# Kernel optimization log

Measured on AMD Instinct MI355X. Metric: run time of the kernel, lower is better.

## Reference

```python
import jax, jax.numpy as jnp
import numpy as np

D_MODEL = 1024
D_FF = 4096
N_HEADS = 16
EPS = 1e-5


def setup_inputs() -> dict:
    key = jax.random.key(0)
    ks = jax.random.split(key, 12)
    s = 0.02
    inp = {
        "x": jax.random.normal(ks[0], (4, 2048, D_MODEL), dtype=jnp.float32),
        "Wq": jax.random.normal(ks[1], (D_MODEL, D_MODEL), dtype=jnp.float32) * s,
        "bq": jnp.zeros((D_MODEL,), jnp.float32),
        "Wk": jax.random.normal(ks[2], (D_MODEL, D_MODEL), dtype=jnp.float32) * s,
        "bk": jnp.zeros((D_MODEL,), jnp.float32),
        "Wv": jax.random.normal(ks[3], (D_MODEL, D_MODEL), dtype=jnp.float32) * s,
        "bv": jnp.zeros((D_MODEL,), jnp.float32),
        "Wo": jax.random.normal(ks[4], (D_MODEL, D_MODEL), dtype=jnp.float32) * s,
        "bo": jnp.zeros((D_MODEL,), jnp.float32),
        "ln1_g": jnp.ones((D_MODEL,), jnp.float32),
        "ln1_b": jnp.zeros((D_MODEL,), jnp.float32),
        "ln2_g": jnp.ones((D_MODEL,), jnp.float32),
        "ln2_b": jnp.zeros((D_MODEL,), jnp.float32),
        "W1": jax.random.normal(ks[5], (D_MODEL, D_FF), dtype=jnp.float32) * s,
        "b1": jnp.zeros((D_FF,), jnp.float32),
        "W2": jax.random.normal(ks[6], (D_FF, D_MODEL), dtype=jnp.float32) * s,
        "b2": jnp.zeros((D_MODEL,), jnp.float32),
    }
    return inp


def _layernorm(x, g, b):
    mu = jnp.mean(x, axis=-1, keepdims=True)
    var = jnp.mean(jnp.square(x - mu), axis=-1, keepdims=True)
    return (x - mu) * jax.lax.rsqrt(var + EPS) * g + b


def _block(x, Wq, bq, Wk, bk, Wv, bv, Wo, bo, ln1_g, ln1_b, ln2_g, ln2_b, W1, b1, W2, b2):
    B, S, D = x.shape
    H = N_HEADS
    dk = D // H
    # --- sub_layer1: LN -> MHA ---
    h = _layernorm(x, ln1_g, ln1_b)
    q = (h @ Wq + bq).reshape(B, S, H, dk).transpose(0, 2, 1, 3)  # [B,H,S,dk]
    k = (h @ Wk + bk).reshape(B, S, H, dk).transpose(0, 2, 1, 3)
    v = (h @ Wv + bv).reshape(B, S, H, dk).transpose(0, 2, 1, 3)
    scores = jnp.einsum('bhqd,bhkd->bhqk', q, k) / jnp.sqrt(jnp.float32(dk))
    attn = jax.nn.softmax(scores, axis=-1)
    o = jnp.einsum('bhqk,bhkd->bhqd', attn, v)  # [B,H,S,dk]
    o = o.transpose(0, 2, 1, 3).reshape(B, S, D)
    x = x + (o @ Wo + bo)
    # --- sub_layer2: LN -> MLP (exact GELU) ---
    h = _layernorm(x, ln2_g, ln2_b)
    h = jax.nn.gelu(h @ W1 + b1, approximate=False)
    x = x + (h @ W2 + b2)
    return x


def reference(x, Wq, bq, Wk, bk, Wv, bv, Wo, bo, ln1_g, ln1_b, ln2_g, ln2_b, W1, b1, W2, b2):
    return _block(x, Wq, bq, Wk, bk, Wv, bv, Wo, bo, ln1_g, ln1_b, ln2_g, ln2_b, W1, b1, W2, b2)
```

## Files before the change

### kernel.cpp

```cpp
#include <hip/hip_runtime.h>
#include <hip/hip_bf16.h>
#include <math.h>

#define DM   1024
#define DFF  4096
#define NHEAD 16
#define DKH  64
#define SEQ  2048
#define NBATCH 4
#define NTOK 8192

typedef __attribute__((ext_vector_type(8))) __bf16 bf16x8;
typedef __attribute__((ext_vector_type(8))) short short8;
typedef __attribute__((ext_vector_type(4))) float f32x4;
typedef __attribute__((ext_vector_type(16))) float f32x16;
typedef __attribute__((ext_vector_type(4))) unsigned int u32x4;
typedef __attribute__((ext_vector_type(4))) unsigned short ushort4v;

__device__ __forceinline__ unsigned short f2bf(float f) {
    unsigned u = __builtin_bit_cast(unsigned, f);
    u += 0x7fffu + ((u >> 16) & 1u);
    return (unsigned short)(u >> 16);
}

__device__ __forceinline__ void gload_lds16(const void* g, void* l) {
    __builtin_amdgcn_global_load_lds(
        (const __attribute__((address_space(1))) unsigned int*)g,
        (__attribute__((address_space(3))) unsigned int*)l, 16, 0, 0);
}

__global__ __launch_bounds__(256) void transpose_cvt(
        const float* __restrict__ src, unsigned short* __restrict__ dst, int R, int C) {
    __shared__ unsigned short tile[32][33];
    const int c0 = blockIdx.x * 32, r0 = blockIdx.y * 32;
    const int tx = threadIdx.x & 31, ty = threadIdx.x >> 5;
    #pragma unroll
    for (int j = 0; j < 32; j += 8)
        tile[ty + j][tx] = f2bf(src[(size_t)(r0 + ty + j) * C + (c0 + tx)]);
    __syncthreads();
    #pragma unroll
    for (int j = 0; j < 32; j += 8)
        dst[(size_t)(c0 + ty + j) * R + (r0 + tx)] = tile[tx][ty + j];
}

__global__ __launch_bounds__(256) void concat_bias(
        const float* __restrict__ a, const float* __restrict__ b,
        const float* __restrict__ c, float* __restrict__ out) {
    int i = blockIdx.x * 256 + threadIdx.x;
    out[i] = (i < 1024) ? a[i] : (i < 2048 ? b[i - 1024] : c[i - 2048]);
}

__global__ __launch_bounds__(256) void ln_kernel(
        const float* __restrict__ x, const float* __restrict__ g,
        const float* __restrict__ b, unsigned short* __restrict__ out) {
    const int row = blockIdx.x, t = threadIdx.x;
    const float4 v = ((const float4*)(x + (size_t)row * DM))[t];
    float s1 = v.x + v.y + v.z + v.w;
    float s2 = v.x * v.x + v.y * v.y + v.z * v.z + v.w * v.w;
    #pragma unroll
    for (int off = 32; off > 0; off >>= 1) {
        s1 += __shfl_xor(s1, off, 64);
        s2 += __shfl_xor(s2, off, 64);
    }
    __shared__ float w1[4], w2[4];
    const int wid = t >> 6, lane = t & 63;
    if (lane == 0) { w1[wid] = s1; w2[wid] = s2; }
    __syncthreads();
    s1 = w1[0] + w1[1] + w1[2] + w1[3];
    s2 = w2[0] + w2[1] + w2[2] + w2[3];
    const float mu = s1 * (1.0f / DM);
    const float rs = rsqrtf(s2 * (1.0f / DM) - mu * mu + 1e-5f);
    const float4 gv = ((const float4*)g)[t];
    const float4 bv = ((const float4*)b)[t];
    ushort4v o;
    o[0] = f2bf((v.x - mu) * rs * gv.x + bv.x);
    o[1] = f2bf((v.y - mu) * rs * gv.y + bv.y);
    o[2] = f2bf((v.z - mu) * rs * gv.z + bv.z);
    o[3] = f2bf((v.w - mu) * rs * gv.w + bv.w);
    *(ushort4v*)(out + (size_t)row * DM + t * 4) = o;
}

template<int EP>
__global__ __launch_bounds__(256) void gemm_bf16(
        const unsigned short* __restrict__ A, const unsigned short* __restrict__ BT,
        const float* __restrict__ bias, const float* __restrict__ res,
        void* __restrict__ outp, int M, int N, int K) {
    const int lane = threadIdx.x & 63;
    const int wid  = threadIdx.x >> 6;
    const int m0 = blockIdx.y * 128;
    const int n0 = blockIdx.x * 128;
    __shared__ short As[128 * 32];
    __shared__ short Bs[128 * 32];
    f32x4 acc[4][4] = {};
    const int wm = wid >> 1, wn = wid & 1;
    const int srow = lane >> 2;
    const int scol = (lane & 3) << 3;

    for (int k0 = 0; k0 < K; k0 += 32) {
        __syncthreads();
        #pragma unroll
        for (int i = 0; i < 2; ++i) {
            const int rt = (wid * 2 + i) * 16;
            gload_lds16(A  + (size_t)(m0 + rt + srow) * K + k0 + scol, &As[(wid * 2 + i) * 512]);
            gload_lds16(BT + (size_t)(n0 + rt + srow) * K + k0 + scol, &Bs[(wid * 2 + i) * 512]);
        }
        __syncthreads();
        bf16x8 af[4], bfr[4];
        #pragma unroll
        for (int mi = 0; mi < 4; ++mi)
            af[mi] = *(const bf16x8*)&As[(wm * 64 + mi * 16 + (lane & 15)) * 32 + ((lane >> 4) << 3)];
        #pragma unroll
        for (int ni = 0; ni < 4; ++ni)
            bfr[ni] = *(const bf16x8*)&Bs[(wn * 64 + ni * 16 + (lane & 15)) * 32 + ((lane >> 4) << 3)];
        #pragma unroll
        for (int mi = 0; mi < 4; ++mi)
            #pragma unroll
            for (int ni = 0; ni < 4; ++ni)
                acc[mi][ni] = __builtin_amdgcn_mfma_f32_16x16x32_bf16(af[mi], bfr[ni], acc[mi][ni], 0, 0, 0);
    }

    const int r_base = m0 + wm * 64 + ((lane >> 4) << 2);
    const int c_base = n0 + wn * 64 + (lane & 15);

    if (EP == 4) {
        unsigned short* qP = (unsigned short*)outp;
        unsigned short* kP = qP + (size_t)NTOK * 1024;
        unsigned short* vP = qP + (size_t)2 * NTOK * 1024;
        const int b  = m0 >> 11;
        const int sb = (m0 & 2047) + wm * 64 + ((lane >> 4) << 2);
        #pragma unroll
        for (int ni = 0; ni < 4; ++ni) {
            const int col = c_base + ni * 16;
            const int which = col >> 10;
            const int h = (col >> 6) & 15;
            const int d = col & 63;
            const float bv = bias[col];
            const size_t bh = (size_t)(b * NHEAD + h);
            if (which < 2) {
                unsigned short* dst = (which ? kP : qP) + bh * SEQ * 64 + d;
                #pragma unroll
                for (int mi = 0; mi < 4; ++mi)
                    #pragma unroll
                    for (int i = 0; i < 4; ++i)
                        dst[(size_t)(sb + mi * 16 + i) * 64] = f2bf(acc[mi][ni][i] + bv);
            } else {
                unsigned short* dst = vP + bh * SEQ * 64;
                #pragma unroll
                for (int mi = 0; mi < 4; ++mi) {
                    const int s0 = sb + mi * 16;
                    ushort4v o;
                    #pragma unroll
                    for (int i = 0; i < 4; ++i) o[i] = f2bf(acc[mi][ni][i] + bv);
                    *(ushort4v*)(dst + (s0 >> 5) * 2048 + d * 32 + (s0 & 31)) = o;
                }
            }
        }
        return;
    }

    #pragma unroll
    for (int ni = 0; ni < 4; ++ni) {
        const int col = c_base + ni * 16;
        const float bv = bias[col];
        #pragma unroll
        for (int mi = 0; mi < 4; ++mi) {
            #pragma unroll
            for (int i = 0; i < 4; ++i) {
                const int row = r_base + mi * 16 + i;
                const size_t idx = (size_t)row * N + col;
                float v = acc[mi][ni][i] + bv;
                if (EP == 1 || EP == 3) v += res[idx];
                if (EP == 2) v = 0.5f * v * (1.0f + erff(v * 0.70710678118f));
                if (EP == 0 || EP == 2) ((unsigned short*)outp)[idx] = f2bf(v);
                else                    ((float*)outp)[idx] = v;
            }
        }
    }
}

__global__ __launch_bounds__(256, 4) void attn_kernel(
        const unsigned short* __restrict__ qP, const unsigned short* __restrict__ kP,
        const unsigned short* __restrict__ vP, unsigned short* __restrict__ o) {
    const int lane = threadIdx.x & 63;
    const int wid  = threadIdx.x >> 6;
    const int l31  = lane & 31;
    const int hi   = lane >> 5;
    const int bh = blockIdx.y;
    const int b = bh >> 4, h = bh & 15;
    const int q0 = blockIdx.x * 128 + wid * 32;

    __shared__ short Ks[2][2048];
    __shared__ short Vs[2][2048];
    __shared__ float lsum[4][32];

    bf16x8 qf[4];
    {
        const unsigned short* qp = qP + ((size_t)bh * SEQ + q0 + l31) * 64 + hi * 8;
        #pragma unroll
        for (int s = 0; s < 4; ++s) qf[s] = *(const bf16x8*)(qp + 16 * s);
    }

    const int krow  = wid * 8 + (lane >> 3);
    const int k_src = krow * 64 + (((lane & 7) ^ (lane >> 3)) << 3);
    const int vrow  = wid * 16 + (lane >> 2);
    const int v_src = vrow * 32 + (((lane & 3) ^ ((vrow >> 1) & 3)) << 3);
    const unsigned short* kb = kP + (size_t)bh * SEQ * 64 + k_src;
    const unsigned short* vb = vP + (size_t)bh * SEQ * 64 + v_src;
    short* ksd = &Ks[0][0] + wid * 512;
    short* vsd = &Vs[0][0] + wid * 512;

    auto STAGE = [&](int buf, int kv0) {
        gload_lds16(kb + (size_t)kv0 * 64, ksd + buf * 2048);
        gload_lds16(vb + (size_t)(kv0 >> 5) * 2048, vsd + buf * 2048);
    };

    STAGE(0, 0);
    asm volatile("s_waitcnt vmcnt(0)" ::: "memory");
    __builtin_amdgcn_s_barrier();

    f32x16 oacc0 = {}, oacc1 = {};
    float m_r = -1e30f, l_r = 0.0f;
    const float CE = 0.18033688011f;

    for (int kv0 = 0; kv0 < SEQ; kv0 += 32) {
        const int cur = (kv0 >> 5) & 1;
        if (kv0 + 32 < SEQ) STAGE(cur ^ 1, kv0 + 32);

        const short* kc = &Ks[cur][0];
        const short* vc = &Vs[cur][0];
        bf16x8 kf[4], vf[2][2];
        #pragma unroll
        for (int s = 0; s < 4; ++s)
            kf[s] = *(const bf16x8*)(kc + l31 * 64 + (((2 * s + hi) ^ (l31 & 7)) << 3));
        #pragma unroll
        for (int s = 0; s < 2; ++s)
            #pragma unroll
            for (int n = 0; n < 2; ++n) {
                const int d = l31 + 32 * n;
                vf[s][n] = *(const bf16x8*)(vc + d * 32 + (((2 * s + hi) ^ ((d >> 1) & 3)) << 3));
            }

        f32x16 S = {};
        #pragma unroll
        for (int s = 0; s < 4; ++s)
            S = __builtin_amdgcn_mfma_f32_32x32x16_bf16(kf[s], qf[s], S, 0, 0, 0);

        float t8[8];
        #pragma unroll
        for (int j = 0; j < 8; ++j) t8[j] = fmaxf(S[j], S[j + 8]);
        float tm = fmaxf(fmaxf(fmaxf(t8[0], t8[4]), fmaxf(t8[1], t8[5])),
                         fmaxf(fmaxf(t8[2], t8[6]), fmaxf(t8[3], t8[7])));
        tm = fmaxf(tm, __shfl_xor(tm, 32, 64));
        if (!__all(tm - m_r <= 44.0f)) {
            const float mn = fmaxf(m_r, tm);
            const float es = exp2f((m_r - mn) * CE);
            l_r *= es;
            #pragma unroll
            for (int r = 0; r < 16; ++r) { oacc0[r] *= es; oacc1[r] *= es; }
            m_r = mn;
        }
        float p[16];
        #pragma unroll
        for (int r = 0; r < 16; ++r) p[r] = exp2f((S[r] - m_r) * CE);
        float a8[8];
        #pragma unroll
        for (int j = 0; j < 8; ++j) a8[j] = p[j] + p[j + 8];
        float rs = ((a8[0] + a8[4]) + (a8[1] + a8[5])) + ((a8[2] + a8[6]) + (a8[3] + a8[7]));
        rs += __shfl_xor(rs, 32, 64);
        l_r += rs;

        unsigned pk[8];
        #pragma unroll
        for (int i = 0; i < 8; ++i) {
            unsigned rr;
            asm("v_cvt_pk_bf16_f32 %0, %1, %2" : "=v"(rr) : "v"(p[2 * i]), "v"(p[2 * i + 1]));
            pk[i] = rr;
        }
        asm volatile("v_permlane32_swap_b32 %0, %1" : "+v"(pk[0]), "+v"(pk[2]));
        asm volatile("v_permlane32_swap_b32 %0, %1" : "+v"(pk[1]), "+v"(pk[3]));
        asm volatile("v_permlane32_swap_b32 %0, %1" : "+v"(pk[4]), "+v"(pk[6]));
        asm volatile("v_permlane32_swap_b32 %0, %1" : "+v"(pk[5]), "+v"(pk[7]));
        const bf16x8 A0 = __builtin_bit_cast(bf16x8, (u32x4){pk[0], pk[1], pk[2], pk[3]});
        const bf16x8 A1 = __builtin_bit_cast(bf16x8, (u32x4){pk[4], pk[5], pk[6], pk[7]});

        oacc0 = __builtin_amdgcn_mfma_f32_32x32x16_bf16(A0, vf[0][0], oacc0, 0, 0, 0);
        oacc1 = __builtin_amdgcn_mfma_f32_32x32x16_bf16(A0, vf[0][1], oacc1, 0, 0, 0);
        oacc0 = __builtin_amdgcn_mfma_f32_32x32x16_bf16(A1, vf[1][0], oacc0, 0, 0, 0);
        oacc1 = __builtin_amdgcn_mfma_f32_32x32x16_bf16(A1, vf[1][1], oacc1, 0, 0, 0);

        asm volatile("s_waitcnt vmcnt(0)" ::: "memory");
        __builtin_amdgcn_s_barrier();
    }

    if (lane < 32) lsum[wid][l31] = 1.0f / l_r;
    float inv[16];
    #pragma unroll
    for (int r = 0; r < 16; ++r)
        inv[r] = lsum[wid][(r & 3) + 8 * (r >> 2) + 4 * hi];

    unsigned short* op = o + (size_t)(b * SEQ + q0) * DM + h * 64 + l31;
    #pragma unroll
    for (int r = 0; r < 16; ++r) {
        const int q = (r & 3) + 8 * (r >> 2) + 4 * hi;
        op[(size_t)q * DM]      = f2bf(oacc0[r] * inv[r]);
        op[(size_t)q * DM + 32] = f2bf(oacc1[r] * inv[r]);
    }
}

extern "C" void kernel_launch(void* const* d_in, const int* in_sizes, int n_in,
                              void* d_out, int out_size, void* d_ws, size_t ws_size,
                              hipStream_t stream) {
    const float* x    = (const float*)d_in[0];
    const float* Wq   = (const float*)d_in[1];
    const float* bq   = (const float*)d_in[2];
    const float* Wk   = (const float*)d_in[3];
    const float* bk   = (const float*)d_in[4];
    const float* Wv   = (const float*)d_in[5];
    const float* bv   = (const float*)d_in[6];
    const float* Wo   = (const float*)d_in[7];
    const float* bo   = (const float*)d_in[8];
    const float* ln1g = (const float*)d_in[9];
    const float* ln1b = (const float*)d_in[10];
    const float* ln2g = (const float*)d_in[11];
    const float* ln2b = (const float*)d_in[12];
    const float* W1   = (const float*)d_in[13];
    const float* b1   = (const float*)d_in[14];
    const float* W2   = (const float*)d_in[15];
    const float* b2   = (const float*)d_in[16];

    char* ws = (char*)d_ws;
    size_t off = 0;
    auto alloc = [&](size_t bytes) {
        char* p = ws + off;
        off = (off + bytes + 255) & ~(size_t)255;
        return p;
    };
    unsigned short* wqkvT = (unsigned short*)alloc((size_t)3072 * 1024 * 2);
    unsigned short* woT   = (unsigned short*)alloc((size_t)1024 * 1024 * 2);
    unsigned short* w1T   = (unsigned short*)alloc((size_t)4096 * 1024 * 2);
    unsigned short* w2T   = (unsigned short*)alloc((size_t)1024 * 4096 * 2);
    float*          bqkv  = (float*)alloc((size_t)3072 * 4);
    unsigned short* hbuf  = (unsigned short*)alloc((size_t)NTOK * DM * 2);
    unsigned short* pack  = (unsigned short*)alloc((size_t)NTOK * 3072 * 2);
    unsigned short* obuf  = (unsigned short*)alloc((size_t)NTOK * DM * 2);
    float*          x2    = (float*)alloc((size_t)NTOK * DM * 4);
    unsigned short* h2    = (unsigned short*)alloc((size_t)NTOK * DM * 2);
    unsigned short* gbuf  = (unsigned short*)alloc((size_t)NTOK * DFF * 2);

    const unsigned short* qP = pack;
    const unsigned short* kP = pack + (size_t)NTOK * 1024;
    const unsigned short* vP = pack + (size_t)2 * NTOK * 1024;

    transpose_cvt<<<dim3(32, 32), 256, 0, stream>>>(Wq, wqkvT,                 1024, 1024);
    transpose_cvt<<<dim3(32, 32), 256, 0, stream>>>(Wk, wqkvT + 1024 * 1024,   1024, 1024);
    transpose_cvt<<<dim3(32, 32), 256, 0, stream>>>(Wv, wqkvT + 2 * 1024 * 1024, 1024, 1024);
    transpose_cvt<<<dim3(32, 32), 256, 0, stream>>>(Wo, woT,                   1024, 1024);
    transpose_cvt<<<dim3(128, 32), 256, 0, stream>>>(W1, w1T, 1024, 4096);
    transpose_cvt<<<dim3(32, 128), 256, 0, stream>>>(W2, w2T, 4096, 1024);
    concat_bias<<<12, 256, 0, stream>>>(bq, bk, bv, bqkv);

    ln_kernel<<<NTOK, 256, 0, stream>>>(x, ln1g, ln1b, hbuf);

    gemm_bf16<4><<<dim3(3072 / 128, NTOK / 128), 256, 0, stream>>>(
        hbuf, wqkvT, bqkv, nullptr, pack, NTOK, 3072, 1024);

    attn_kernel<<<dim3(SEQ / 128, NBATCH * NHEAD), 256, 0, stream>>>(qP, kP, vP, obuf);

    gemm_bf16<1><<<dim3(1024 / 128, NTOK / 128), 256, 0, stream>>>(
        obuf, woT, bo, x, x2, NTOK, 1024, 1024);

    ln_kernel<<<NTOK, 256, 0, stream>>>(x2, ln2g, ln2b, h2);

    gemm_bf16<2><<<dim3(4096 / 128, NTOK / 128), 256, 0, stream>>>(
        h2, w1T, b1, nullptr, gbuf, NTOK, 4096, 1024);

    gemm_bf16<3><<<dim3(1024 / 128, NTOK / 128), 256, 0, stream>>>(
        gbuf, w2T, b2, x2, d_out, NTOK, 1024, 4096);

    (void)in_sizes; (void)n_in; (void)out_size; (void)ws_size;
}
```

Measured before the change: 631.9 us.

## Replace GEMM with 8-wave double-buffered, swizzled, software-pipelined MFMA kernel

Measured after the change: 613.5 us. 2.9% less time.

```diff
diff --git a/kernel.cpp b/kernel.cpp
--- a/kernel.cpp
+++ b/kernel.cpp
@@ -80,56 +80,142 @@
     *(ushort4v*)(out + (size_t)row * DM + t * 4) = o;
 }
 
-template<int EP>
-__global__ __launch_bounds__(256) void gemm_bf16(
+#define LGKM0 do { asm volatile("s_waitcnt lgkmcnt(0)" ::: "memory"); \
+                   __builtin_amdgcn_sched_barrier(0); } while (0)
+#define SB0   __builtin_amdgcn_sched_barrier(0)
+
+template<int BM, int BN, int EP>
+__global__ __launch_bounds__(512, 2) void gemm8p(
         const unsigned short* __restrict__ A, const unsigned short* __restrict__ BT,
         const float* __restrict__ bias, const float* __restrict__ res,
         void* __restrict__ outp, int M, int N, int K) {
-    const int lane = threadIdx.x & 63;
-    const int wid  = threadIdx.x >> 6;
-    const int m0 = blockIdx.y * 128;
-    const int n0 = blockIdx.x * 128;
-    __shared__ short As[128 * 32];
-    __shared__ short Bs[128 * 32];
-    f32x4 acc[4][4] = {};
-    const int wm = wid >> 1, wn = wid & 1;
-    const int srow = lane >> 2;
-    const int scol = (lane & 3) << 3;
-
-    for (int k0 = 0; k0 < K; k0 += 32) {
-        __syncthreads();
-        #pragma unroll
-        for (int i = 0; i < 2; ++i) {
-            const int rt = (wid * 2 + i) * 16;
-            gload_lds16(A  + (size_t)(m0 + rt + srow) * K + k0 + scol, &As[(wid * 2 + i) * 512]);
-            gload_lds16(BT + (size_t)(n0 + rt + srow) * K + k0 + scol, &Bs[(wid * 2 + i) * 512]);
-        }
-        __syncthreads();
-        bf16x8 af[4], bfr[4];
-        #pragma unroll
-        for (int mi = 0; mi < 4; ++mi)
-            af[mi] = *(const bf16x8*)&As[(wm * 64 + mi * 16 + (lane & 15)) * 32 + ((lane >> 4) << 3)];
-        #pragma unroll
-        for (int ni = 0; ni < 4; ++ni)
-            bfr[ni] = *(const bf16x8*)&Bs[(wn * 64 + ni * 16 + (lane & 15)) * 32 + ((lane >> 4) << 3)];
-        #pragma unroll
-        for (int mi = 0; mi < 4; ++mi)
+    constexpr int WM = BM / 2, WN = BN / 4;
+    constexpr int MR = WM / 16, NR = WN / 16;
+    constexpr int MH = MR / 2;
+    constexpr int LA = BM / 64, LB = BN / 64;
+
+    const int t = threadIdx.x;
+    const int lane = t & 63, wid = t >> 6;
+    const int wr = wid >> 2, wc = wid & 3;
+    const int m0 = blockIdx.y * BM, n0 = blockIdx.x * BN;
+    const int NT = K >> 6;
+
+    __shared__ alignas(16) short As[2 * BM * 64];
+    __shared__ alignas(16) short Bs[2 * BN * 64];
+
+    const int srow = t >> 3, schk = t & 7;
+    const int sw = ((schk ^ (srow & 7)) << 3);
+    const unsigned short* gA = A  + (size_t)(m0 + srow) * K + (schk << 3);
+    const unsigned short* gB = BT + (size_t)(n0 + srow) * K + (schk << 3);
+
+    bf16x8 rA[LA], rB[LB];
+    bf16x8 fa[MH][2], fb[4][2];
+    f32x4 acc[MR][NR] = {};
+
+    auto LOADA = [&](int tile) {
+        const unsigned short* p = gA + tile * 64;
+        #pragma unroll
+        for (int j = 0; j < LA; ++j) rA[j] = *(const bf16x8*)(p + (size_t)j * 64 * K);
+    };
+    auto LOADB = [&](int tile) {
+        const unsigned short* p = gB + tile * 64;
+        #pragma unroll
+        for (int j = 0; j < LB; ++j) rB[j] = *(const bf16x8*)(p + (size_t)j * 64 * K);
+    };
+    auto WRA = [&](int q) {
+        short* d = As + q * (BM * 64) + srow * 64 + sw;
+        #pragma unroll
+        for (int j = 0; j < LA; ++j) *(bf16x8*)(d + j * 4096) = rA[j];
+    };
+    auto WRB = [&](int q) {
+        short* d = Bs + q * (BN * 64) + srow * 64 + sw;
+        #pragma unroll
+        for (int j = 0; j < LB; ++j) *(bf16x8*)(d + j * 4096) = rB[j];
+    };
+    auto RDA = [&](int p, int mh) {
+        const short* base = As + p * (BM * 64);
+        #pragma unroll
+        for (int m = 0; m < MH; ++m) {
+            const int row = wr * WM + (mh * MH + m) * 16 + (lane & 15);
             #pragma unroll
-            for (int ni = 0; ni < 4; ++ni)
-                acc[mi][ni] = __builtin_amdgcn_mfma_f32_16x16x32_bf16(af[mi], bfr[ni], acc[mi][ni], 0, 0, 0);
-    }
-
-    const int r_base = m0 + wm * 64 + ((lane >> 4) << 2);
-    const int c_base = n0 + wn * 64 + (lane & 15);
-
-    if (EP == 4) {
+            for (int kk = 0; kk < 2; ++kk)
+                fa[m][kk] = *(const bf16x8*)(base + row * 64 +
+                    ((((kk << 2) | (lane >> 4)) ^ (lane & 7)) << 3));
+        }
+    };
+    auto RDB = [&](int p, int nh) {
+        const short* base = Bs + p * (BN * 64);
+        #pragma unroll
+        for (int n = 0; n < 2; ++n) {
+            const int row = wc * WN + (nh * 2 + n) * 16 + (lane & 15);
+            #pragma unroll
+            for (int kk = 0; kk < 2; ++kk)
+                fb[nh * 2 + n][kk] = *(const bf16x8*)(base + row * 64 +
+                    ((((kk << 2) | (lane >> 4)) ^ (lane & 7)) << 3));
+        }
+    };
+
+#define MMA(mh, nh)                                                            \
+    do {                                                                       \
+        _Pragma("unroll")                                                      \
+        for (int m_ = 0; m_ < MH; ++m_)                                        \
+            _Pragma("unroll")                                                  \
+            for (int n_ = 0; n_ < 2; ++n_)                                     \
+                _Pragma("unroll")                                              \
+                for (int kk_ = 0; kk_ < 2; ++kk_)                              \
+                    acc[(mh) * MH + m_][(nh) * 2 + n_] =                       \
+                        __builtin_amdgcn_mfma_f32_16x16x32_bf16(               \
+                            fa[m_][kk_], fb[(nh) * 2 + n_][kk_],               \
+                            acc[(mh) * MH + m_][(nh) * 2 + n_], 0, 0, 0);      \
+    } while (0)
+
+    LOADA(0); SB0; LOADB(0);
+    asm volatile("s_waitcnt vmcnt(0)" ::: "memory");
+    WRA(0); WRB(0);
+    LOADA(NT > 1 ? 1 : 0); SB0; LOADB(NT > 1 ? 1 : 0);
+    asm volatile("s_waitcnt lgkmcnt(0)" ::: "memory");
+    SB0;
+    __builtin_amdgcn_s_barrier();
+    asm volatile("" ::: "memory");
+
+    for (int tt = 0; tt < NT; ++tt) {
+        const int p = tt & 1, q = p ^ 1;
+        const int tp2 = (tt + 2 < NT) ? tt + 2 : NT - 1;
+        RDA(p, 0); RDB(p, 0);
+        LGKM0;
+        __builtin_amdgcn_s_setprio(1); MMA(0, 0); __builtin_amdgcn_s_setprio(0);
+        RDB(p, 1);
+        asm volatile("s_waitcnt vmcnt(4)" ::: "memory");
+        WRA(q);
+        LGKM0;
+        LOADA(tp2);
+        SB0;
+        __builtin_amdgcn_s_setprio(1); MMA(0, 1); __builtin_amdgcn_s_setprio(0);
+        RDA(p, 1);
+        if constexpr (LA == 4) { asm volatile("s_waitcnt vmcnt(4)" ::: "memory"); }
+        else                   { asm volatile("s_waitcnt vmcnt(2)" ::: "memory"); }
+        WRB(q);
+        LGKM0;
+        LOADB(tp2);
+        SB0;
+        __builtin_amdgcn_s_setprio(1); MMA(1, 1); __builtin_amdgcn_s_setprio(0);
+        __builtin_amdgcn_s_setprio(1); MMA(1, 0); __builtin_amdgcn_s_setprio(0);
+        __builtin_amdgcn_s_barrier();
+        asm volatile("" ::: "memory");
+    }
+#undef MMA
+
+    const int r_base = m0 + wr * WM + ((lane >> 4) << 2);
+    const int c_base = n0 + wc * WN + (lane & 15);
+
+    if constexpr (EP == 4) {
         unsigned short* qP = (unsigned short*)outp;
         unsigned short* kP = qP + (size_t)NTOK * 1024;
         unsigned short* vP = qP + (size_t)2 * NTOK * 1024;
         const int b  = m0 >> 11;
-        const int sb = (m0 & 2047) + wm * 64 + ((lane >> 4) << 2);
-        #pragma unroll
-        for (int ni = 0; ni < 4; ++ni) {
+        const int sb = (m0 & 2047) + wr * WM + ((lane >> 4) << 2);
+        #pragma unroll
+        for (int ni = 0; ni < NR; ++ni) {
             const int col = c_base + ni * 16;
             const int which = col >> 10;
             const int h = (col >> 6) & 15;
@@ -139,14 +225,14 @@
             if (which < 2) {
                 unsigned short* dst = (which ? kP : qP) + bh * SEQ * 64 + d;
                 #pragma unroll
-                for (int mi = 0; mi < 4; ++mi)
+                for (int mi = 0; mi < MR; ++mi)
                     #pragma unroll
                     for (int i = 0; i < 4; ++i)
                         dst[(size_t)(sb + mi * 16 + i) * 64] = f2bf(acc[mi][ni][i] + bv);
             } else {
                 unsigned short* dst = vP + bh * SEQ * 64;
                 #pragma unroll
-                for (int mi = 0; mi < 4; ++mi) {
+                for (int mi = 0; mi < MR; ++mi) {
                     const int s0 = sb + mi * 16;
                     ushort4v o;
                     #pragma unroll
@@ -159,11 +245,11 @@
     }
 
     #pragma unroll
-    for (int ni = 0; ni < 4; ++ni) {
+    for (int ni = 0; ni < NR; ++ni) {
         const int col = c_base + ni * 16;
         const float bv = bias[col];
         #pragma unroll
-        for (int mi = 0; mi < 4; ++mi) {
+        for (int mi = 0; mi < MR; ++mi) {
             #pragma unroll
             for (int i = 0; i < 4; ++i) {
                 const int row = r_base + mi * 16 + i;
@@ -361,20 +447,20 @@
 
     ln_kernel<<<NTOK, 256, 0, stream>>>(x, ln1g, ln1b, hbuf);
 
-    gemm_bf16<4><<<dim3(3072 / 128, NTOK / 128), 256, 0, stream>>>(
+    gemm8p<256, 256, 4><<<dim3(3072 / 256, NTOK / 256), 512, 0, stream>>>(
         hbuf, wqkvT, bqkv, nullptr, pack, NTOK, 3072, 1024);
 
     attn_kernel<<<dim3(SEQ / 128, NBATCH * NHEAD), 256, 0, stream>>>(qP, kP, vP, obuf);
 
-    gemm_bf16<1><<<dim3(1024 / 128, NTOK / 128), 256, 0, stream>>>(
+    gemm8p<128, 256, 1><<<dim3(1024 / 256, NTOK / 128), 512, 0, stream>>>(
         obuf, woT, bo, x, x2, NTOK, 1024, 1024);
 
     ln_kernel<<<NTOK, 256, 0, stream>>>(x2, ln2g, ln2b, h2);
 
-    gemm_bf16<2><<<dim3(4096 / 128, NTOK / 128), 256, 0, stream>>>(
+    gemm8p<256, 256, 2><<<dim3(4096 / 256, NTOK / 256), 512, 0, stream>>>(
         h2, w1T, b1, nullptr, gbuf, NTOK, 4096, 1024);
 
-    gemm_bf16<3><<<dim3(1024 / 128, NTOK / 128), 256, 0, stream>>>(
+    gemm8p<128, 256, 3><<<dim3(1024 / 256, NTOK / 128), 512, 0, stream>>>(
         gbuf, w2T, b2, x2, d_out, NTOK, 1024, 4096);
 
     (void)in_sizes; (void)n_in; (void)out_size; (void)ws_size;
```
